# Optimization experiments

Measured on AMD Instinct MI355X. Metric: run time of the kernel, lower is better.

Reference implementation:

```python
import jax, jax.numpy as jnp
import numpy as np

EPS = 1e-12

def squash(s):
    # standard capsule squash: ||s||^2/(1+||s||^2) * s/||s||
    n2 = jnp.sum(s * s, axis=-1, keepdims=True)
    return n2 / (1.0 + n2) * s / jnp.sqrt(n2 + EPS)

def setup_inputs() -> dict:
    key = jax.random.key(0)
    k1, k2 = jax.random.split(key)
    B, O, I, DOUT, DIN = 64, 32, 2048, 16, 16
    u = jax.random.normal(k1, (B, I, DIN), dtype=jnp.float32)
    # TruncatedNormal(stddev=0.1) init for W
    W = 0.1 * jax.random.truncated_normal(k2, -2.0, 2.0, (1, O, I, DOUT, DIN), dtype=jnp.float32)
    bias = jnp.full((1, O, DOUT), 0.1, dtype=jnp.float32)
    return {"u": u, "W": W, "bias": bias}

def reference(u, W, bias):
    routing_iterations = 3
    O = W.shape[1]
    # u: [B, I, DIN], W: [1, O, I, DOUT, DIN]
    u_norm = jnp.linalg.norm(u, axis=-1)                     # [B, I]
    # u_hat[b,o,i,d] = sum_k W[0,o,i,d,k] * u[b,i,k]  (batched matmul instead of tile+mul+sum)
    u_hat = jnp.einsum('oidk,bik->boid', W[0], u)            # [B, O, I, DOUT]
    u_hat_norm = jnp.linalg.norm(u_hat, axis=-1, keepdims=True)   # [B, O, I, 1]
    new_u_hat_norm = jnp.minimum(u_hat_norm, u_norm[:, None, :, None])
    u_hat = u_hat / (u_hat_norm + EPS) * new_u_hat_norm

    B = u.shape[0]
    b_ij = jnp.zeros((B, O, u.shape[1], 1), dtype=u.dtype)
    t_const = jnp.float32(np.log(0.9 * (O - 1)) - np.log(1.0 - 0.9))
    v_j = None
    c_ij = None
    for r in range(routing_iterations):
        c_ij = jax.nn.softmax(b_ij, axis=1)                  # softmax over out capsules
        s_j = jnp.sum(c_ij * u_hat, axis=2) + bias           # [B, O, DOUT]
        v_j = squash(s_j)
        if r < routing_iterations - 1:
            # gamma-routing agreement: distance between prediction and output
            d = jnp.linalg.norm(v_j[:, :, None, :] - u_hat, axis=-1, keepdims=True)  # [B,O,I,1]
            d_o = jnp.mean(d)
            d_p = d_o * 0.5
            t = t_const / (d_p - d_o + 1e-12)
            b_ij = t * d
    return (v_j, c_ij)
```

## Files before the change

kernel.cpp:

```cpp
#include <hip/hip_runtime.h>
#include <hip/hip_bf16.h>
#include <hip/hip_fp16.h>
#include <math.h>

#define BB 64
#define OO 32
#define II 2048
#define DD 16
#define CAPS_EPS 1e-12f
#define T_CONST 5.6312118f

#define TIS 16
#define SLEN 16
#define NSTRIP 128

#define OFF_DSUM  0ULL
#define OFF_V     16ULL
#define OFF_UNORM 32784ULL
#define OFF_UBF   163856ULL
#define OFF_Y     1212432ULL
#define OFF_DD    34766864ULL
#define OFF_TMAX  38961168ULL
#define OFF_TDEN  39092240ULL
#define OFF_PART  39223312ULL

typedef __attribute__((ext_vector_type(8))) short bf16x8;
typedef __attribute__((ext_vector_type(4))) float f32x4;

union AU { bf16x8 v; unsigned short h[8]; uint4 u4; };
union YU { __half h[4]; uint2 u2; };
union YL { uint4 u4[2]; __half h[16]; };

__device__ __forceinline__ unsigned short f2bf(float x) {
    __hip_bfloat16 h = __float2bfloat16(x);
    unsigned short s; __builtin_memcpy(&s, &h, 2); return s;
}

__global__ __launch_bounds__(256) void uprep_kernel(
    const float* __restrict__ u, float* __restrict__ ws)
{
    const int gid = blockIdx.x * 256 + threadIdx.x;
    if (gid < 2) ws[OFF_DSUM + gid] = 0.f;
    const int i = gid >> 6, b = gid & 63;

    const float4* up = reinterpret_cast<const float4*>(u + ((size_t)b * II + i) * DD);
    float4 t0 = up[0], t1 = up[1], t2 = up[2], t3 = up[3];
    float un2 = t0.x*t0.x + t0.y*t0.y + t0.z*t0.z + t0.w*t0.w
              + t1.x*t1.x + t1.y*t1.y + t1.z*t1.z + t1.w*t1.w
              + t2.x*t2.x + t2.y*t2.y + t2.z*t2.z + t2.w*t2.w
              + t3.x*t3.x + t3.y*t3.y + t3.z*t3.z + t3.w*t3.w;
    ws[OFF_UNORM + (size_t)i * 64 + b] = __builtin_amdgcn_sqrtf(un2);

    AU a0, a1;
    a0.h[0]=f2bf(t0.x); a0.h[1]=f2bf(t0.y); a0.h[2]=f2bf(t0.z); a0.h[3]=f2bf(t0.w);
    a0.h[4]=f2bf(t1.x); a0.h[5]=f2bf(t1.y); a0.h[6]=f2bf(t1.z); a0.h[7]=f2bf(t1.w);
    a1.h[0]=f2bf(t2.x); a1.h[1]=f2bf(t2.y); a1.h[2]=f2bf(t2.z); a1.h[3]=f2bf(t2.w);
    a1.h[4]=f2bf(t3.x); a1.h[5]=f2bf(t3.y); a1.h[6]=f2bf(t3.z); a1.h[7]=f2bf(t3.w);
    unsigned short* ubf = (unsigned short*)(ws + OFF_UBF);
    uint4* dst = reinterpret_cast<uint4*>(ubf + ((size_t)i * 64 + b) * 16);
    dst[0] = a0.u4; dst[1] = a1.u4;
}

__global__ __launch_bounds__(256) void s0w_kernel(
    const float* __restrict__ W, float* __restrict__ ws)
{
    const int strip = blockIdx.x;
    const int og   = blockIdx.y;
    const int wave = threadIdx.x >> 6;
    const int lane = threadIdx.x & 63;
    const int o    = og * 4 + wave;
    const int q    = lane >> 4;
    const int n    = lane & 15;

    const unsigned short* ubf = (const unsigned short*)(ws + OFF_UBF);
    const float* unorm = ws + OFF_UNORM;
    __half* Y = (__half*)(ws + OFF_Y);
    float* part = ws + OFF_PART;

    f32x4 s_acc[4];
    #pragma unroll
    for (int g = 0; g < 4; ++g) s_acc[g] = (f32x4){0.f, 0.f, 0.f, 0.f};

    for (int ii = 0; ii < TIS; ++ii) {
        const int i = strip * TIS + ii;

        AU au; au.u4 = make_uint4(0, 0, 0, 0);
        if (q < 2) {
            const float* wp = W + (((size_t)o * II + i) * 16 + n) * 16 + q * 8;
            float4 w0 = *(const float4*)(wp);
            float4 w1 = *(const float4*)(wp + 4);
            au.h[0]=f2bf(w0.x); au.h[1]=f2bf(w0.y); au.h[2]=f2bf(w0.z); au.h[3]=f2bf(w0.w);
            au.h[4]=f2bf(w1.x); au.h[5]=f2bf(w1.y); au.h[6]=f2bf(w1.z); au.h[7]=f2bf(w1.w);
        }

        f32x4 d4[4];
        #pragma unroll
        for (int g = 0; g < 4; ++g) {
            AU bu;
            bu.u4 = *reinterpret_cast<const uint4*>(
                ubf + ((size_t)i * 64 + g * 16 + n) * 16 + (q & 1) * 8);
            d4[g] = __builtin_amdgcn_mfma_f32_16x16x32_bf16(
                au.v, bu.v, (f32x4){0.f, 0.f, 0.f, 0.f}, 0, 0, 0);
        }

        #pragma unroll
        for (int g = 0; g < 4; ++g) {
            float n2 = d4[g][0]*d4[g][0] + d4[g][1]*d4[g][1]
                     + d4[g][2]*d4[g][2] + d4[g][3]*d4[g][3];
            n2 += __shfl_xor(n2, 16);
            n2 += __shfl_xor(n2, 32);
            const float rsq  = __builtin_amdgcn_rsqf(n2 + CAPS_EPS);
            const float rawn = n2 * rsq;
            const float un = unorm[(size_t)i * 64 + g * 16 + n];
            const float scale = fminf(rawn, un) * rsq;

            YU yu;
            yu.h[0] = __float2half(scale * d4[g][0]);
            yu.h[1] = __float2half(scale * d4[g][1]);
            yu.h[2] = __float2half(scale * d4[g][2]);
            yu.h[3] = __float2half(scale * d4[g][3]);
            *reinterpret_cast<uint2*>(
                Y + (((size_t)i * OO + o) * 64 + g * 16 + n) * 16 + q * 4) = yu.u2;

            const float cs = 0.03125f * scale;
            s_acc[g][0] += cs * d4[g][0];
            s_acc[g][1] += cs * d4[g][1];
            s_acc[g][2] += cs * d4[g][2];
            s_acc[g][3] += cs * d4[g][3];
        }
    }

    #pragma unroll
    for (int g = 0; g < 4; ++g) {
        float4 v = make_float4(s_acc[g][0], s_acc[g][1], s_acc[g][2], s_acc[g][3]);
        *reinterpret_cast<float4*>(
            part + (((size_t)strip * OO + o) * 64 + g * 16 + n) * 16 + q * 4) = v;
    }
}

__global__ __launch_bounds__(256) void finv_kernel(
    const float* __restrict__ part, const float* __restrict__ bias,
    float* __restrict__ vout)
{
    const int tid = blockIdx.x * 256 + threadIdx.x;
    const int b = tid >> 9, o = (tid >> 4) & 31, d = tid & 15;
    const size_t base = ((size_t)o * 64 + b) * 16 + d;
    float s = 0.f;
    #pragma unroll 4
    for (int st = 0; st < NSTRIP; ++st)
        s += part[(size_t)st * (OO * 64 * 16) + base];
    s += bias[tid & 511];
    float n2 = s * s;
    #pragma unroll
    for (int off = 1; off < 16; off <<= 1) n2 += __shfl_xor(n2, off);
    vout[tid] = s * n2 * __builtin_amdgcn_rcpf(1.f + n2)
                  * __builtin_amdgcn_rsqf(n2 + CAPS_EPS);
}

template<int SLOT>
__global__ __launch_bounds__(256) void dpass_kernel(float* __restrict__ ws)
{
    const int strip = blockIdx.x;
    const int og    = blockIdx.y;
    const int wave  = threadIdx.x >> 6;
    const int b     = threadIdx.x & 63;
    const int o     = og * 4 + wave;

    const __half* Y   = (const __half*)(ws + OFF_Y);
    const float* v_ws = ws + OFF_V;
    float* dws = ws + OFF_DD;

    float v[16];
    float vn2 = 0.f;
    #pragma unroll
    for (int k = 0; k < 16; ++k) {
        v[k] = v_ws[((size_t)b * OO + o) * 16 + k];
        vn2 += v[k] * v[k];
    }

    float acc = 0.f;
    #pragma unroll 4
    for (int s = 0; s < SLEN; ++s) {
        const int i = strip * SLEN + s;
        const uint4* yp = reinterpret_cast<const uint4*>(
            Y + (((size_t)i * OO + o) * 64 + b) * 16);
        YL yl;
        yl.u4[0] = yp[0];
        yl.u4[1] = yp[1];
        float dot = 0.f, yn2 = 0.f;
        #pragma unroll
        for (int k = 0; k < 16; ++k) {
            const float y = __half2float(yl.h[k]);
            dot += v[k] * y;
            yn2 += y * y;
        }
        const float dd2 = fmaxf(vn2 - 2.f * dot + yn2, 0.f);
        const float dist = __builtin_amdgcn_sqrtf(dd2);
        dws[((size_t)i * OO + o) * 64 + b] = dist;
        acc += dist;
    }

    #pragma unroll
    for (int off = 32; off > 0; off >>= 1) acc += __shfl_down(acc, off);
    __shared__ float red[4];
    if ((threadIdx.x & 63) == 0) red[wave] = acc;
    __syncthreads();
    if (threadIdx.x == 0)
        atomicAdd(&ws[OFF_DSUM + SLOT], red[0] + red[1] + red[2] + red[3]);
}

template<int SLOT>
__global__ __launch_bounds__(256) void csoft_kernel(float* __restrict__ ws)
{
    const int gid = blockIdx.x * 256 + threadIdx.x;
    const int i = gid >> 6, b = gid & 63;

    const float* dws = ws + OFF_DD;
    const float dsum = ws[OFF_DSUM + SLOT];
    const float tval = T_CONST * __builtin_amdgcn_rcpf(
        -0.5f * dsum * (1.0f / 4194304.0f) + 1e-12f);

    float dv[OO];
    #pragma unroll
    for (int o = 0; o < OO; ++o)
        dv[o] = tval * dws[((size_t)i * OO + o) * 64 + b];
    float m = -1e30f;
    #pragma unroll
    for (int o = 0; o < OO; ++o) m = fmaxf(m, dv[o]);
    float den = 0.f;
    #pragma unroll
    for (int o = 0; o < OO; ++o) den += __expf(dv[o] - m);
    ws[OFF_TMAX + (size_t)i * 64 + b] = m;
    ws[OFF_TDEN + (size_t)i * 64 + b] = den;
}

template<int SLOT>
__global__ __launch_bounds__(256) void spass_kernel(float* __restrict__ ws)
{
    const int strip = blockIdx.x;
    const int og    = blockIdx.y;
    const int wave  = threadIdx.x >> 6;
    const int b     = threadIdx.x & 63;
    const int o     = og * 4 + wave;

    const __half* Y = (const __half*)(ws + OFF_Y);
    const float* dws  = ws + OFF_DD;
    const float* tmax = ws + OFF_TMAX;
    const float* tden = ws + OFF_TDEN;
    float* part = ws + OFF_PART;

    const float dsum = ws[OFF_DSUM + SLOT];
    const float tval = T_CONST * __builtin_amdgcn_rcpf(
        -0.5f * dsum * (1.0f / 4194304.0f) + 1e-12f);

    float acc[16];
    #pragma unroll
    for (int k = 0; k < 16; ++k) acc[k] = 0.f;

    #pragma unroll 4
    for (int s = 0; s < SLEN; ++s) {
        const int i = strip * SLEN + s;
        const uint4* yp = reinterpret_cast<const uint4*>(
            Y + (((size_t)i * OO + o) * 64 + b) * 16);
        YL yl;
        yl.u4[0] = yp[0];
        yl.u4[1] = yp[1];
        const float d  = dws[((size_t)i * OO + o) * 64 + b];
        const float m  = tmax[(size_t)i * 64 + b];
        const float dn = tden[(size_t)i * 64 + b];
        const float p = __expf(tval * d - m) * __builtin_amdgcn_rcpf(dn);
        #pragma unroll
        for (int k = 0; k < 16; ++k)
            acc[k] += p * __half2float(yl.h[k]);
    }

    float* pp = part + (((size_t)strip * OO + o) * 64 + b) * 16;
    *reinterpret_cast<float4*>(pp +  0) = make_float4(acc[0],  acc[1],  acc[2],  acc[3]);
    *reinterpret_cast<float4*>(pp +  4) = make_float4(acc[4],  acc[5],  acc[6],  acc[7]);
    *reinterpret_cast<float4*>(pp +  8) = make_float4(acc[8],  acc[9],  acc[10], acc[11]);
    *reinterpret_cast<float4*>(pp + 12) = make_float4(acc[12], acc[13], acc[14], acc[15]);
}

__global__ __launch_bounds__(256) void transpose_kernel(
    const float* __restrict__ ws, float* __restrict__ dst)
{
    __shared__ float tile[32][65];
    const float* dws  = ws + OFF_DD;
    const float* tmax = ws + OFF_TMAX;
    const float* tden = ws + OFF_TDEN;
    const float dsum = ws[OFF_DSUM + 1];
    const float tval = T_CONST * __builtin_amdgcn_rcpf(
        -0.5f * dsum * (1.0f / 4194304.0f) + 1e-12f);

    const int o  = blockIdx.y;
    const int i0 = blockIdx.x * 32;
    #pragma unroll
    for (int k = 0; k < 8; ++k) {
        const int lin = k * 256 + threadIdx.x;
        const int r = lin >> 6, b = lin & 63;
        const int i = i0 + r;
        const float d = dws[((size_t)i * OO + o) * 64 + b];
        tile[r][b] = __expf(tval * d - tmax[(size_t)i * 64 + b])
                   * __builtin_amdgcn_rcpf(tden[(size_t)i * 64 + b]);
    }
    __syncthreads();
    #pragma unroll
    for (int k = 0; k < 8; ++k) {
        const int lin = k * 256 + threadIdx.x;
        const int b = lin >> 5, r = lin & 31;
        dst[((size_t)b * OO + o) * II + i0 + r] = tile[r][b];
    }
}

extern "C" void kernel_launch(void* const* d_in, const int* in_sizes, int n_in,
                              void* d_out, int out_size, void* d_ws, size_t ws_size,
                              hipStream_t stream) {
    const float* u    = (const float*)d_in[0];
    const float* W    = (const float*)d_in[1];
    const float* bias = (const float*)d_in[2];
    float* out = (float*)d_out;
    float* ws  = (float*)d_ws;

    float* v_ws = ws + OFF_V;
    float* part = ws + OFF_PART;
    float* cout = out + (size_t)BB * OO * DD;

    dim3 blk(256);
    dim3 grid_s(NSTRIP, 8);

    uprep_kernel<<<512, blk, 0, stream>>>(u, ws);
    s0w_kernel<<<grid_s, blk, 0, stream>>>(W, ws);
    finv_kernel<<<128, blk, 0, stream>>>(part, bias, v_ws);
    dpass_kernel<0><<<grid_s, blk, 0, stream>>>(ws);
    csoft_kernel<0><<<512, blk, 0, stream>>>(ws);
    spass_kernel<0><<<grid_s, blk, 0, stream>>>(ws);
    finv_kernel<<<128, blk, 0, stream>>>(part, bias, v_ws);
    dpass_kernel<1><<<grid_s, blk, 0, stream>>>(ws);
    csoft_kernel<1><<<512, blk, 0, stream>>>(ws);
    spass_kernel<1><<<grid_s, blk, 0, stream>>>(ws);
    finv_kernel<<<128, blk, 0, stream>>>(part, bias, out);
    transpose_kernel<<<dim3(64, 32), blk, 0, stream>>>(ws, cout);
}
```

Measured before the change: 326.5 us.

## Store distances and partial sums in fp16 and software-prefetch Y in routing passes

Distances and the per-strip partial sums are now stored as fp16 instead of fp32. Together with the smaller intermediate buffers, this is meant to halve the memory traffic for those arrays across the d-pass, softmax, s-pass, finalize and transpose kernels. The d-pass and s-pass loops are fully unrolled with explicit one-step-ahead register prefetch of the next Y row and its softmax statistics, to hide load latency. The cost is reduced precision in the routing distances and in the accumulated sums, which could shift the softmax outputs.

```diff
diff --git a/kernel.cpp b/kernel.cpp
--- a/kernel.cpp
+++ b/kernel.cpp
@@ -20,9 +20,9 @@
 #define OFF_UBF   163856ULL
 #define OFF_Y     1212432ULL
 #define OFF_DD    34766864ULL
-#define OFF_TMAX  38961168ULL
-#define OFF_TDEN  39092240ULL
-#define OFF_PART  39223312ULL
+#define OFF_TMAX  36864016ULL
+#define OFF_TDEN  36995088ULL
+#define OFF_PART  37126160ULL
 
 typedef __attribute__((ext_vector_type(8))) short bf16x8;
 typedef __attribute__((ext_vector_type(4))) float f32x4;
@@ -30,6 +30,8 @@
 union AU { bf16x8 v; unsigned short h[8]; uint4 u4; };
 union YU { __half h[4]; uint2 u2; };
 union YL { uint4 u4[2]; __half h[16]; };
+union PS { __half h[16]; uint4 u4[2]; };
+union P4 { __half h[4]; uint2 u2; };
 
 __device__ __forceinline__ unsigned short f2bf(float x) {
     __hip_bfloat16 h = __float2bfloat16(x);
@@ -75,7 +77,7 @@
     const unsigned short* ubf = (const unsigned short*)(ws + OFF_UBF);
     const float* unorm = ws + OFF_UNORM;
     __half* Y = (__half*)(ws + OFF_Y);
-    float* part = ws + OFF_PART;
+    __half* part_h = (__half*)(ws + OFF_PART);
 
     f32x4 s_acc[4];
     #pragma unroll
@@ -132,9 +134,13 @@
 
     #pragma unroll
     for (int g = 0; g < 4; ++g) {
-        float4 v = make_float4(s_acc[g][0], s_acc[g][1], s_acc[g][2], s_acc[g][3]);
-        *reinterpret_cast<float4*>(
-            part + (((size_t)strip * OO + o) * 64 + g * 16 + n) * 16 + q * 4) = v;
+        P4 pu;
+        pu.h[0] = __float2half(s_acc[g][0]);
+        pu.h[1] = __float2half(s_acc[g][1]);
+        pu.h[2] = __float2half(s_acc[g][2]);
+        pu.h[3] = __float2half(s_acc[g][3]);
+        *reinterpret_cast<uint2*>(
+            part_h + (((size_t)strip * OO + o) * 64 + g * 16 + n) * 16 + q * 4) = pu.u2;
     }
 }
 
@@ -144,11 +150,12 @@
 {
     const int tid = blockIdx.x * 256 + threadIdx.x;
     const int b = tid >> 9, o = (tid >> 4) & 31, d = tid & 15;
+    const __half* part_h = (const __half*)part;
     const size_t base = ((size_t)o * 64 + b) * 16 + d;
     float s = 0.f;
     #pragma unroll 4
     for (int st = 0; st < NSTRIP; ++st)
-        s += part[(size_t)st * (OO * 64 * 16) + base];
+        s += __half2float(part_h[(size_t)st * (OO * 64 * 16) + base]);
     s += bias[tid & 511];
     float n2 = s * s;
     #pragma unroll
@@ -168,25 +175,31 @@
 
     const __half* Y   = (const __half*)(ws + OFF_Y);
     const float* v_ws = ws + OFF_V;
-    float* dws = ws + OFF_DD;
+    __half* dws = (__half*)(ws + OFF_DD);
 
     float v[16];
     float vn2 = 0.f;
-    #pragma unroll
-    for (int k = 0; k < 16; ++k) {
-        v[k] = v_ws[((size_t)b * OO + o) * 16 + k];
-        vn2 += v[k] * v[k];
-    }
+    const float* vp = v_ws + ((size_t)b * OO + o) * 16;
+    #pragma unroll
+    for (int k = 0; k < 16; ++k) { v[k] = vp[k]; vn2 += v[k] * v[k]; }
+
+    const size_t istride = (size_t)OO * 64 * 16;
+    const __half* ybase = Y + ((size_t)(strip * SLEN) * OO + o) * 64 * 16
+                            + (size_t)b * 16;
 
     float acc = 0.f;
-    #pragma unroll 4
+    uint4 c0 = *reinterpret_cast<const uint4*>(ybase);
+    uint4 c1 = *reinterpret_cast<const uint4*>(ybase + 8);
+
+    #pragma unroll
     for (int s = 0; s < SLEN; ++s) {
-        const int i = strip * SLEN + s;
-        const uint4* yp = reinterpret_cast<const uint4*>(
-            Y + (((size_t)i * OO + o) * 64 + b) * 16);
-        YL yl;
-        yl.u4[0] = yp[0];
-        yl.u4[1] = yp[1];
+        uint4 n0, n1;
+        if (s + 1 < SLEN) {
+            const __half* np = ybase + (size_t)(s + 1) * istride;
+            n0 = *reinterpret_cast<const uint4*>(np);
+            n1 = *reinterpret_cast<const uint4*>(np + 8);
+        }
+        YL yl; yl.u4[0] = c0; yl.u4[1] = c1;
         float dot = 0.f, yn2 = 0.f;
         #pragma unroll
         for (int k = 0; k < 16; ++k) {
@@ -195,9 +208,11 @@
             yn2 += y * y;
         }
         const float dd2 = fmaxf(vn2 - 2.f * dot + yn2, 0.f);
-        const float dist = __builtin_amdgcn_sqrtf(dd2);
-        dws[((size_t)i * OO + o) * 64 + b] = dist;
-        acc += dist;
+        const __half dh = __float2half(__builtin_amdgcn_sqrtf(dd2));
+        const int i = strip * SLEN + s;
+        dws[((size_t)i * OO + o) * 64 + b] = dh;
+        acc += __half2float(dh);
+        if (s + 1 < SLEN) { c0 = n0; c1 = n1; }
     }
 
     #pragma unroll
@@ -215,7 +230,7 @@
     const int gid = blockIdx.x * 256 + threadIdx.x;
     const int i = gid >> 6, b = gid & 63;
 
-    const float* dws = ws + OFF_DD;
+    const __half* dws = (const __half*)(ws + OFF_DD);
     const float dsum = ws[OFF_DSUM + SLOT];
     const float tval = T_CONST * __builtin_amdgcn_rcpf(
         -0.5f * dsum * (1.0f / 4194304.0f) + 1e-12f);
@@ -223,7 +238,7 @@
     float dv[OO];
     #pragma unroll
     for (int o = 0; o < OO; ++o)
-        dv[o] = tval * dws[((size_t)i * OO + o) * 64 + b];
+        dv[o] = tval * __half2float(dws[((size_t)i * OO + o) * 64 + b]);
     float m = -1e30f;
     #pragma unroll
     for (int o = 0; o < OO; ++o) m = fmaxf(m, dv[o]);
@@ -244,48 +259,63 @@
     const int o     = og * 4 + wave;
 
     const __half* Y = (const __half*)(ws + OFF_Y);
-    const float* dws  = ws + OFF_DD;
+    const __half* dws = (const __half*)(ws + OFF_DD);
     const float* tmax = ws + OFF_TMAX;
     const float* tden = ws + OFF_TDEN;
-    float* part = ws + OFF_PART;
+    __half* part_h = (__half*)(ws + OFF_PART);
 
     const float dsum = ws[OFF_DSUM + SLOT];
     const float tval = T_CONST * __builtin_amdgcn_rcpf(
         -0.5f * dsum * (1.0f / 4194304.0f) + 1e-12f);
 
+    const size_t istride = (size_t)OO * 64 * 16;
+    const int i0 = strip * SLEN;
+    const __half* ybase = Y + ((size_t)i0 * OO + o) * 64 * 16 + (size_t)b * 16;
+
     float acc[16];
     #pragma unroll
     for (int k = 0; k < 16; ++k) acc[k] = 0.f;
 
-    #pragma unroll 4
+    uint4 c0 = *reinterpret_cast<const uint4*>(ybase);
+    uint4 c1 = *reinterpret_cast<const uint4*>(ybase + 8);
+    float dcur = __half2float(dws[((size_t)i0 * OO + o) * 64 + b]);
+    float mcur = tmax[(size_t)i0 * 64 + b];
+    float ncur = tden[(size_t)i0 * 64 + b];
+
+    #pragma unroll
     for (int s = 0; s < SLEN; ++s) {
-        const int i = strip * SLEN + s;
-        const uint4* yp = reinterpret_cast<const uint4*>(
-            Y + (((size_t)i * OO + o) * 64 + b) * 16);
-        YL yl;
-        yl.u4[0] = yp[0];
-        yl.u4[1] = yp[1];
-        const float d  = dws[((size_t)i * OO + o) * 64 + b];
-        const float m  = tmax[(size_t)i * 64 + b];
-        const float dn = tden[(size_t)i * 64 + b];
-        const float p = __expf(tval * d - m) * __builtin_amdgcn_rcpf(dn);
+        uint4 n0, n1; float dnx = 0.f, mnx = 0.f, nnx = 1.f;
+        if (s + 1 < SLEN) {
+            const int in = i0 + s + 1;
+            const __half* np = ybase + (size_t)(s + 1) * istride;
+            n0 = *reinterpret_cast<const uint4*>(np);
+            n1 = *reinterpret_cast<const uint4*>(np + 8);
+            dnx = __half2float(dws[((size_t)in * OO + o) * 64 + b]);
+            mnx = tmax[(size_t)in * 64 + b];
+            nnx = tden[(size_t)in * 64 + b];
+        }
+        YL yl; yl.u4[0] = c0; yl.u4[1] = c1;
+        const float p = __expf(tval * dcur - mcur) * __builtin_amdgcn_rcpf(ncur);
         #pragma unroll
         for (int k = 0; k < 16; ++k)
             acc[k] += p * __half2float(yl.h[k]);
-    }
-
-    float* pp = part + (((size_t)strip * OO + o) * 64 + b) * 16;
-    *reinterpret_cast<float4*>(pp +  0) = make_float4(acc[0],  acc[1],  acc[2],  acc[3]);
-    *reinterpret_cast<float4*>(pp +  4) = make_float4(acc[4],  acc[5],  acc[6],  acc[7]);
-    *reinterpret_cast<float4*>(pp +  8) = make_float4(acc[8],  acc[9],  acc[10], acc[11]);
-    *reinterpret_cast<float4*>(pp + 12) = make_float4(acc[12], acc[13], acc[14], acc[15]);
+        if (s + 1 < SLEN) { c0 = n0; c1 = n1; dcur = dnx; mcur = mnx; ncur = nnx; }
+    }
+
+    PS su;
+    #pragma unroll
+    for (int k = 0; k < 16; ++k) su.h[k] = __float2half(acc[k]);
+    uint4* pp = reinterpret_cast<uint4*>(
+        part_h + (((size_t)strip * OO + o) * 64 + b) * 16);
+    pp[0] = su.u4[0];
+    pp[1] = su.u4[1];
 }
 
 __global__ __launch_bounds__(256) void transpose_kernel(
     const float* __restrict__ ws, float* __restrict__ dst)
 {
     __shared__ float tile[32][65];
-    const float* dws  = ws + OFF_DD;
+    const __half* dws = (const __half*)(ws + OFF_DD);
     const float* tmax = ws + OFF_TMAX;
     const float* tden = ws + OFF_TDEN;
     const float dsum = ws[OFF_DSUM + 1];
@@ -299,7 +329,7 @@
         const int lin = k * 256 + threadIdx.x;
         const int r = lin >> 6, b = lin & 63;
         const int i = i0 + r;
-        const float d = dws[((size_t)i * OO + o) * 64 + b];
+        const float d = __half2float(dws[((size_t)i * OO + o) * 64 + b]);
         tile[r][b] = __expf(tval * d - tmax[(size_t)i * 64 + b])
                    * __builtin_amdgcn_rcpf(tden[(size_t)i * 64 + b]);
     }
```

After: 334.5 us. +2.5%, slower.
